# Kernel optimization log

Measured on AMD Instinct MI355X. Metric: run time of the kernel, lower is better.

## Reference

```python
import jax, jax.numpy as jnp
import numpy as np

BATCH, SEQ_LEN, ENC_IN = 16, 1024, 12
N_HIPPO, MODES, OUT_DIM = 256, 32, 5
MULTISCALE = [1, 2, 4]
EPS_VAR, EPS_AFF = 1e-5, 1e-10


def _transition_lmu(N):
    Q = np.arange(N, dtype=np.float64)
    R = (2 * Q + 1)[:, None]
    j, i = np.meshgrid(Q, Q)
    A = np.where(i < j, -1.0, (-1.0) ** (i - j + 1)) * R
    B = (-1.0) ** Q[:, None] * R
    return A, B


def _bilinear_discretize(A, B, dt):
    # scipy.signal.cont2discrete(..., method='bilinear')
    N = A.shape[0]
    I = np.eye(N)
    ima = I - (dt / 2.0) * A
    Ad = np.linalg.solve(ima, I + (dt / 2.0) * A)
    Bd = np.linalg.solve(ima, dt * B)
    return Ad, Bd.squeeze(-1)


def _eval_legendre(N, x):
    # P_n(x) for n=0..N-1 via three-term recurrence; returns (len(x), N)
    P = np.zeros((len(x), N), dtype=np.float64)
    P[:, 0] = 1.0
    if N > 1:
        P[:, 1] = x
    for n in range(1, N - 1):
        P[:, n + 1] = ((2 * n + 1) * x * P[:, n] - n * P[:, n - 1]) / (n + 1)
    return P


def setup_inputs() -> dict:
    key = jax.random.key(0)
    ks = jax.random.split(key, 8)
    A_list, B_list, E_list = [], [], []
    for mult in MULTISCALE:
        dt = 1.0 / SEQ_LEN / mult
        A, B = _transition_lmu(N_HIPPO)
        Ad, Bd = _bilinear_discretize(A, B, dt)
        vals = np.arange(0.0, 1.0, dt)
        ev = _eval_legendre(N_HIPPO, 1.0 - 2.0 * vals)  # (seq_len*mult, N)
        A_list.append(Ad); B_list.append(Bd); E_list.append(ev[-SEQ_LEN:, :])
    scale = 1.0 / (N_HIPPO * N_HIPPO)
    inp = {
        "x_enc": jax.random.normal(ks[0], (BATCH, SEQ_LEN, ENC_IN), jnp.float32),
        "affine_w": jnp.ones((1, 1, ENC_IN), jnp.float32),
        "affine_b": jnp.zeros((1, 1, ENC_IN), jnp.float32),
        "w_spec_re": scale * jax.random.uniform(ks[1], (len(MULTISCALE), N_HIPPO, N_HIPPO, MODES), jnp.float32),
        "w_spec_im": scale * jax.random.uniform(ks[2], (len(MULTISCALE), N_HIPPO, N_HIPPO, MODES), jnp.float32),
        "w_mlp": 0.3 * jax.random.normal(ks[3], (1, len(MULTISCALE)), jnp.float32),
        "b_mlp": jnp.zeros((1,), jnp.float32),
        "w_fc": 0.05 * jax.random.normal(ks[4], (OUT_DIM, ENC_IN), jnp.float32),
        "b_fc": jnp.zeros((OUT_DIM,), jnp.float32),
        "A_mats": jnp.asarray(np.stack(A_list), jnp.float32),   # (3, N, N)
        "B_vecs": jnp.asarray(np.stack(B_list), jnp.float32),   # (3, N)
        "eval_last": jnp.asarray(np.stack(E_list), jnp.float32),  # (3, seq_len, N)
    }
    return inp


def reference(x_enc, affine_w, affine_b, w_spec_re, w_spec_im, w_mlp, b_mlp,
              w_fc, b_fc, A_mats, B_vecs, eval_last):
    L = x_enc.shape[1]
    # RevIN-style normalization (means/stdev are detached in torch)
    means = jax.lax.stop_gradient(jnp.mean(x_enc, axis=1, keepdims=True))
    xc = x_enc - means
    stdev = jax.lax.stop_gradient(jnp.sqrt(jnp.var(xc, axis=1, keepdims=True) + EPS_VAR))
    x = xc / stdev * affine_w + affine_b          # (B, L, C)
    xt = jnp.transpose(x, (0, 2, 1))              # (B, C, L)
    xt_seq = jnp.moveaxis(xt, -1, 0)              # (L, B, C)
    w_spec = (w_spec_re + 1j * w_spec_im).astype(jnp.complex64)
    modes2 = w_spec.shape[-1]
    decs = []
    for s in range(len(MULTISCALE)):
        A, Bv = A_mats[s], B_vecs[s]
        def step(c, f):  # c: (B,C,N), f: (B,C)
            c = c @ A.T + f[..., None] * Bv
            return c, c
        c0 = jnp.zeros(xt.shape[:2] + (A.shape[0],), xt.dtype)
        _, cs = jax.lax.scan(step, c0, xt_seq)    # (L, B, C, N)
        x_in_c = jnp.transpose(cs, (1, 2, 3, 0))  # (B, C, N, L)
        x_ft = jnp.fft.rfft(x_in_c)               # (B, C, N, L//2+1)
        out_low = jnp.einsum('bjix,iox->bjox', x_ft[..., :modes2], w_spec[s])
        out_ft = jnp.pad(out_low, ((0, 0), (0, 0), (0, 0), (0, x_ft.shape[-1] - modes2)))
        out = jnp.fft.irfft(out_ft, n=L)          # (B, C, N, L)
        x_dec_c = out[..., L - 1]                 # (B, C, N)
        decs.append(x_dec_c @ eval_last[s].T)     # (B, C, L)
    xd = jnp.stack(decs, axis=-1)                 # (B, C, L, 3)
    xd = (xd @ w_mlp.T + b_mlp)[..., 0]           # (B, C, L)
    x_dec = jnp.transpose(xd, (0, 2, 1))          # (B, L, C)
    x_dec = (x_dec - affine_b) / (affine_w + EPS_AFF) * stdev + means
    feat = jnp.mean(jnp.transpose(x_dec, (0, 2, 1)), axis=-1)  # (B, C)
    return feat @ w_fc.T + b_fc                   # (B, OUT_DIM)
```

## Files before the change

kernel.cpp:

```cpp
#include <hip/hip_runtime.h>
#include <math.h>

#define LSEQ 1024
#define NB 16
#define NC 12
#define NH 256
#define NM 32
#define NS 3
#define TWO_PI 6.283185307179586f

#define NPL   8
#define PSTR  196608
#define VPSTR 786432

#define OFF_MEANS 0
#define OFF_STDEV 192
#define OFF_EPART 384
#define OFF_WT_RE 24960
#define OFF_WT_IM 49536
#define OFF_VP    74112
#define OFF_V     6365568
#define OFF_PP0   7152000
#define OFF_PP1   8724864
#define OFF_H     10297728

__device__ __forceinline__ float block_reduce_sum(float v, float* sbuf) {
  int t = threadIdx.x;
  sbuf[t] = v; __syncthreads();
  for (int off = 128; off > 0; off >>= 1) {
    if (t < off) sbuf[t] += sbuf[t + off];
    __syncthreads();
  }
  float r = sbuf[0];
  __syncthreads();
  return r;
}

__global__ __launch_bounds__(256) void k_front(const float* __restrict__ Bv,
                                               const float* __restrict__ ev,
                                               const float* __restrict__ b_fc,
                                               float* __restrict__ epart,
                                               float* __restrict__ Vp,
                                               float* __restrict__ H,
                                               float* __restrict__ out) {
  int blk = blockIdx.x;
  int t = threadIdx.x;
  if (blk < 96) {
    int s = blk >> 5, ch = blk & 31;
    float acc = 0.f;
    const float* base = ev + (size_t)s * LSEQ * NH + (size_t)ch * 32 * NH + t;
    for (int l = 0; l < 32; ++l) acc += base[(size_t)l * NH];
    epart[(size_t)blk * NH + t] = acc;
  } else if (blk == 96) {
    for (int pl = 0; pl < NPL; ++pl)
      for (int row = t; row < 768; row += 256)
        Vp[(size_t)pl * VPSTR + (size_t)row * LSEQ] = (pl == 0) ? Bv[row] : 0.0f;
  } else {
    for (int e = 0; e < 4; ++e) H[t + 256 * e] = 0.0f;
    if (t < NB * 5) out[t] = b_fc[t % 5];
  }
}

__device__ __forceinline__ void wtilde_task(int w, float* smem,
                                            const float* __restrict__ wre,
                                            const float* __restrict__ wim,
                                            const float* __restrict__ epart,
                                            float* __restrict__ wt_re,
                                            float* __restrict__ wt_im) {
  int s = w >> 8, i = w & 255;
  int t = threadIdx.x;
  float* ebs = smem;
  float* sr  = smem + 256;
  float* si2 = smem + 1280;
  float eb = 0.f;
  for (int ch = 0; ch < 32; ++ch) eb += epart[(s * 32 + ch) * 256 + t];
  ebs[t] = eb * (1.0f / LSEQ);
  __syncthreads();
  const float* br = wre + (size_t)(s * NH + i) * NH * NM;
  const float* bi = wim + (size_t)(s * NH + i) * NH * NM;
  float aR[4] = {0.f, 0.f, 0.f, 0.f}, aI[4] = {0.f, 0.f, 0.f, 0.f};
  #pragma unroll
  for (int it = 0; it < 8; ++it) {
    int o = (t >> 3) + 32 * it;
    float e = ebs[o];
    float4 vr = *(const float4*)(br + (size_t)t * 4 + 1024 * it);
    float4 vi = *(const float4*)(bi + (size_t)t * 4 + 1024 * it);
    aR[0] += e * vr.x; aR[1] += e * vr.y; aR[2] += e * vr.z; aR[3] += e * vr.w;
    aI[0] += e * vi.x; aI[1] += e * vi.y; aI[2] += e * vi.z; aI[3] += e * vi.w;
  }
  *(float4*)(sr + t * 4)  = make_float4(aR[0], aR[1], aR[2], aR[3]);
  *(float4*)(si2 + t * 4) = make_float4(aI[0], aI[1], aI[2], aI[3]);
  __syncthreads();
  if (t < 32) {
    float r = 0.f, im = 0.f;
    #pragma unroll
    for (int og = 0; og < 32; ++og) { r += sr[og * 32 + t]; im += si2[og * 32 + t]; }
    wt_re[(size_t)(s * NM + t) * NH + i] = r;
    wt_im[(size_t)(s * NM + t) * NH + i] = im;
  }
  __syncthreads();
}

#define FMA_ROW(r, av) { acc[r][0] += (av)*b4.x; acc[r][1] += (av)*b4.y; acc[r][2] += (av)*b4.z; acc[r][3] += (av)*b4.w; }

template<int ANP, int BNP>
__device__ __forceinline__ void gemm32(float* As, float* Bs,
                       const float* Abase, int apstr,
                       const float* Bbase, int bpstr, int bld, int colLimit,
                       int rowbase, int colbase, int kb,
                       float* outp, int outld, int outcol0, int outColLim) {
  const int tid = threadIdx.x;
  const int tx = tid & 15, ty = tid >> 4;
  const int kkA = tid & 31, rA = tid >> 5;
  const int jB = tid & 63, kB = tid >> 6;
  float acc[8][4];
  #pragma unroll
  for (int i = 0; i < 8; ++i)
    #pragma unroll
    for (int j = 0; j < 4; ++j) acc[i][j] = 0.f;

  #pragma unroll
  for (int p = 0; p < 16; ++p) {
    int row = rowbase + rA + 8 * p;
    float pv[ANP];
    #pragma unroll
    for (int pp = 0; pp < ANP; ++pp)
      pv[pp] = Abase[(size_t)pp * apstr + (size_t)row * 256 + kb + kkA];
    float v = pv[0];
    #pragma unroll
    for (int pp = 1; pp < ANP; ++pp) v += pv[pp];
    As[kkA * 132 + rA + 8 * p] = v;
  }
  #pragma unroll
  for (int q = 0; q < 8; ++q) {
    int kk = kB + 4 * q;
    int j = colbase + jB;
    float v = 0.f;
    if (j < colLimit) {
      float pv[BNP];
      #pragma unroll
      for (int pp = 0; pp < BNP; ++pp)
        pv[pp] = Bbase[(size_t)pp * bpstr + (size_t)(kb + kk) * bld + j];
      v = pv[0];
      #pragma unroll
      for (int pp = 1; pp < BNP; ++pp) v += pv[pp];
    }
    Bs[kk * 68 + jB] = v;
  }
  __syncthreads();
  #pragma unroll
  for (int kk = 0; kk < 32; ++kk) {
    float4 b4 = *(const float4*)(Bs + kk * 68 + tx * 4);
    float4 a0 = *(const float4*)(As + kk * 132 + ty * 8);
    float4 a1 = *(const float4*)(As + kk * 132 + ty * 8 + 4);
    FMA_ROW(0, a0.x) FMA_ROW(1, a0.y) FMA_ROW(2, a0.z) FMA_ROW(3, a0.w)
    FMA_ROW(4, a1.x) FMA_ROW(5, a1.y) FMA_ROW(6, a1.z) FMA_ROW(7, a1.w)
  }
  __syncthreads();
  if (colbase + 64 <= outColLim) {
    #pragma unroll
    for (int i = 0; i < 8; ++i) {
      int row = rowbase + ty * 8 + i;
      float4 st; st.x = acc[i][0]; st.y = acc[i][1]; st.z = acc[i][2]; st.w = acc[i][3];
      *(float4*)(outp + (size_t)row * outld + outcol0 + colbase + tx * 4) = st;
    }
  } else {
    #pragma unroll
    for (int i = 0; i < 8; ++i) {
      int row = rowbase + ty * 8 + i;
      #pragma unroll
      for (int j = 0; j < 4; ++j) {
        int c = colbase + tx * 4 + j;
        if (c < outColLim) outp[(size_t)row * outld + outcol0 + c] = acc[i][j];
      }
    }
  }
}

template<int ANP>
__global__ __launch_bounds__(256) void k_chain(const float* __restrict__ Pc,
                                               float* __restrict__ Pn,
                                               float* __restrict__ Vp,
                                               int m, int nSq, int ntct,
                                               const float* __restrict__ wre,
                                               const float* __restrict__ wim,
                                               const float* __restrict__ epart,
                                               float* __restrict__ wt_re,
                                               float* __restrict__ wt_im,
                                               int wstart, int wcount,
                                               const float* __restrict__ x,
                                               float* __restrict__ means,
                                               float* __restrict__ stdev,
                                               int statCount, int redCount,
                                               float* __restrict__ V) {
  __shared__ float smem[6608];
  float* As = smem;
  float* Bs = smem + 4224;
  const int blk = blockIdx.x;
  const int t = threadIdx.x;
  const int nExt = 48 * ntct;
  const int b0 = nSq + nExt;
  if (blk < nSq) {
    int slice = blk & 7, rest = blk >> 3;
    int t8 = rest & 7, s = rest >> 3;
    int rt = t8 & 1, ct = t8 >> 1;
    const float* Ab = Pc + (size_t)s * 65536;
    gemm32<ANP, ANP>(As, Bs, Ab, PSTR, Ab, PSTR, 256, 256,
           rt * 128, ct * 64, slice * 32,
           Pn + (size_t)slice * PSTR + (size_t)s * 65536, 256, 0, 256);
  } else if (blk < b0) {
    int e = blk - nSq;
    int slice = e & 7, rt = (e >> 3) & 1, rest2 = e >> 4;
    int ct = rest2 % ntct, s = rest2 / ntct;
    gemm32<ANP, NPL>(As, Bs, Pc + (size_t)s * 65536, PSTR,
           Vp + (size_t)s * 262144, VPSTR, 1024, m,
           rt * 128, ct * 64, slice * 32,
           Vp + (size_t)slice * VPSTR + (size_t)s * 262144, 1024, m, m);
  } else if (blk < b0 + wcount) {
    wtilde_task(wstart + (blk - b0), smem, wre, wim, epart, wt_re, wt_im);
  } else if (blk < b0 + wcount + statCount) {
    int bc = blk - b0 - wcount;
    int b = bc / NC, c = bc % NC;
    float* xs = smem;
    float* red = smem + 1024;
    for (int e = 0; e < 4; ++e) {
      int tau = t + 256 * e;
      xs[tau] = x[((size_t)b * LSEQ + tau) * NC + c];
    }
    __syncthreads();
    float p = 0.f;
    for (int e = 0; e < 4; ++e) p += xs[t + 256 * e];
    float sum = block_reduce_sum(p, red);
    float mean = sum * (1.0f / LSEQ);
    float q = 0.f;
    for (int e = 0; e < 4; ++e) { float d = xs[t + 256 * e] - mean; q += d * d; }
    float sq = block_reduce_sum(q, red);
    if (t == 0) {
      means[bc] = mean;
      stdev[bc] = sqrtf(sq * (1.0f / LSEQ) + 1e-5f);
    }
  } else if (blk < b0 + wcount + statCount + redCount) {
    int rid = blk - b0 - wcount - statCount;
    for (int e = 0; e < 2; ++e) {
      size_t idx = (size_t)rid * 1024 + e * 256 + t;
      float v = 0.f;
      #pragma unroll
      for (int pl = 0; pl < NPL; ++pl) v += Vp[(size_t)pl * VPSTR + idx];
      V[idx] = v;
    }
  }
}

__global__ __launch_bounds__(256) void k_reduceV2(const float* __restrict__ Vp,
                                                  float* __restrict__ V) {
  int t = threadIdx.x;
  for (int e = 0; e < 2; ++e) {
    size_t idx = (size_t)blockIdx.x * 1024 + 512 + e * 256 + t;
    float v = 0.f;
    #pragma unroll
    for (int pl = 0; pl < NPL; ++pl) v += Vp[(size_t)pl * VPSTR + idx];
    V[idx] = v;
  }
}

__global__ __launch_bounds__(256) void k_utscan(const float* __restrict__ wt_re,
                                                const float* __restrict__ wt_im,
                                                const float* __restrict__ V,
                                                const float* __restrict__ w_mlp,
                                                float* __restrict__ H) {
  int blk = blockIdx.x;
  int s = blk / NM, k = blk & 31;
  int t = threadIdx.x;
  __shared__ float sr[LSEQ], si_[LSEQ];
  __shared__ float cr[256], ci[256];
  const float* wr = wt_re + (size_t)blk * NH;
  const float* wi_ = wt_im + (size_t)blk * NH;
  const float* Vs = V + (size_t)s * NH * LSEQ;
  float ar[4] = {0.f, 0.f, 0.f, 0.f}, ai[4] = {0.f, 0.f, 0.f, 0.f};
  for (int i = 0; i < NH; ++i) {
    float a = wr[i], b = wi_[i];
    const float* vrow = Vs + (size_t)i * LSEQ + t;
    #pragma unroll
    for (int e = 0; e < 4; ++e) {
      float v = vrow[256 * e];
      ar[e] += a * v; ai[e] += b * v;
    }
  }
  for (int e = 0; e < 4; ++e) {
    int d = t + 256 * e;
    int frac = (k * d) & 1023;
    float ang = -(TWO_PI / 1024.0f) * (float)frac;
    float sn, csn; sincosf(ang, &sn, &csn);
    sr[d] = ar[e] * csn - ai[e] * sn;
    si_[d] = ar[e] * sn + ai[e] * csn;
  }
  __syncthreads();
  float lr[4], li[4], rr = 0.f, ii = 0.f;
  for (int e = 0; e < 4; ++e) {
    rr += sr[4 * t + e]; ii += si_[4 * t + e];
    lr[e] = rr; li[e] = ii;
  }
  cr[t] = rr; ci[t] = ii;
  __syncthreads();
  for (int off = 1; off < 256; off <<= 1) {
    float pr = 0.f, pi = 0.f;
    if (t >= off) { pr = cr[t - off]; pi = ci[t - off]; }
    __syncthreads();
    cr[t] += pr; ci[t] += pi;
    __syncthreads();
  }
  float offr = (t > 0) ? cr[t - 1] : 0.0f;
  float offi = (t > 0) ? ci[t - 1] : 0.0f;
  for (int e = 0; e < 4; ++e) {
    sr[4 * t + e] = lr[e] + offr;
    si_[4 * t + e] = li[e] + offi;
  }
  __syncthreads();
  float wm = w_mlp[s];
  float coef = wm * ((k == 0) ? 1.0f : 2.0f) * (1.0f / LSEQ);
  for (int e = 0; e < 4; ++e) {
    int tau = t + 256 * e;
    int mIdx = 1023 - tau;
    int frac = (k * (tau + 1)) & 1023;
    float ang = -(TWO_PI / 1024.0f) * (float)frac;
    float sn, csn; sincosf(ang, &sn, &csn);
    float val = coef * (sr[mIdx] * csn - si_[mIdx] * sn);
    atomicAdd(&H[tau], val);
  }
}

__global__ __launch_bounds__(256) void k_feat(const float* __restrict__ x,
                                              const float* __restrict__ means,
                                              const float* __restrict__ stdev,
                                              const float* __restrict__ aw,
                                              const float* __restrict__ ab,
                                              const float* __restrict__ b_mlp,
                                              const float* __restrict__ H,
                                              const float* __restrict__ w_fc,
                                              float* __restrict__ out) {
  int bc = blockIdx.x; int b = bc / NC, c = bc % NC;
  __shared__ float red[256];
  int t = threadIdx.x;
  float mn = means[bc], sd = stdev[bc];
  float w = aw[c], bb = ab[c];
  float acc = 0.f;
  for (int e = 0; e < 4; ++e) {
    int tau = t + 256 * e;
    float xv = x[((size_t)b * LSEQ + tau) * NC + c];
    float f = (xv - mn) / sd * w + bb;
    acc += f * H[tau];
  }
  float sum = block_reduce_sum(acc, red);
  if (t == 0) {
    float mr = sum + b_mlp[0];
    float featv = (mr - bb) / (w + 1e-10f) * sd + mn;
    #pragma unroll
    for (int d = 0; d < 5; ++d)
      atomicAdd(&out[b * 5 + d], featv * w_fc[d * NC + c]);
  }
}

extern "C" void kernel_launch(void* const* d_in, const int* in_sizes, int n_in,
                              void* d_out, int out_size, void* d_ws, size_t ws_size,
                              hipStream_t stream) {
  const float* x_enc   = (const float*)d_in[0];
  const float* aw      = (const float*)d_in[1];
  const float* ab      = (const float*)d_in[2];
  const float* wre     = (const float*)d_in[3];
  const float* wim     = (const float*)d_in[4];
  const float* w_mlp   = (const float*)d_in[5];
  const float* b_mlp   = (const float*)d_in[6];
  const float* w_fc    = (const float*)d_in[7];
  const float* b_fc    = (const float*)d_in[8];
  const float* A_mats  = (const float*)d_in[9];
  const float* B_vecs  = (const float*)d_in[10];
  const float* ev      = (const float*)d_in[11];

  float* ws    = (float*)d_ws;
  float* means = ws + OFF_MEANS;
  float* stdev = ws + OFF_STDEV;
  float* epart = ws + OFF_EPART;
  float* wt_re = ws + OFF_WT_RE;
  float* wt_im = ws + OFF_WT_IM;
  float* Vp    = ws + OFF_VP;
  float* V     = ws + OFF_V;
  float* PP0   = ws + OFF_PP0;
  float* PP1   = ws + OFF_PP1;
  float* H     = ws + OFF_H;
  float* out   = (float*)d_out;

  k_front<<<98, 256, 0, stream>>>(B_vecs, ev, b_fc, epart, Vp, H, out);

  static const int wst[5] = {0, 154, 308, 462, 616};
  static const int wcn[5] = {154, 154, 154, 154, 152};
  const float* Pc = A_mats;
  float* Pn = PP0;
  for (int si = 0; si < 10; ++si) {
    int m = 1 << si;
    int doSq = (si < 9);
    int nSq = doSq ? 192 : 0;
    int ntct = (m + 63) >> 6;
    int wstart = (si < 5) ? wst[si] : 0;
    int wcount = (si < 5) ? wcn[si] : 0;
    int statCount = (si == 0) ? 192 : 0;
    int redCount = (si == 9) ? 768 : 0;
    int grid = nSq + 48 * ntct + wcount + statCount + redCount;
    if (si == 0)
      k_chain<1><<<grid, 256, 0, stream>>>(Pc, Pn, Vp, m, nSq, ntct,
          wre, wim, epart, wt_re, wt_im, wstart, wcount,
          x_enc, means, stdev, statCount, redCount, V);
    else
      k_chain<NPL><<<grid, 256, 0, stream>>>(Pc, Pn, Vp, m, nSq, ntct,
          wre, wim, epart, wt_re, wt_im, wstart, wcount,
          x_enc, means, stdev, statCount, redCount, V);
    if (doSq) { Pc = Pn; Pn = (Pn == PP0) ? PP1 : PP0; }
  }

  k_reduceV2<<<768, 256, 0, stream>>>(Vp, V);
  k_utscan<<<NS * NM, 256, 0, stream>>>(wt_re, wt_im, V, w_mlp, H);
  k_feat<<<192, 256, 0, stream>>>(x_enc, means, stdev, aw, ab, b_mlp, H, w_fc, out);
}
```

Measured before the change: 172.8 us.

## Fold front-end setup into first chain launch and vectorize utscan loads

Removes the separate k_front launch. Its Legendre-sum, H/out init and Vp seeding work now runs as extra block roles inside the first k_chain launch, where columns 0 and 1 of V are computed directly with a small matrix-vector product instead of a GEMM extension. The wtilde tasks are shifted one step later so they read epart only after it has been produced. k_utscan now loads V with float4 and does the twiddle multiply in registers, skipping one shared-memory pass and a barrier. This saves one kernel launch and some shared traffic, but it changes V's column-to-thread mapping and adds more block roles to the chain kernel.

```diff
diff --git a/kernel.cpp b/kernel.cpp
--- a/kernel.cpp
+++ b/kernel.cpp
@@ -34,31 +34,6 @@
   float r = sbuf[0];
   __syncthreads();
   return r;
-}
-
-__global__ __launch_bounds__(256) void k_front(const float* __restrict__ Bv,
-                                               const float* __restrict__ ev,
-                                               const float* __restrict__ b_fc,
-                                               float* __restrict__ epart,
-                                               float* __restrict__ Vp,
-                                               float* __restrict__ H,
-                                               float* __restrict__ out) {
-  int blk = blockIdx.x;
-  int t = threadIdx.x;
-  if (blk < 96) {
-    int s = blk >> 5, ch = blk & 31;
-    float acc = 0.f;
-    const float* base = ev + (size_t)s * LSEQ * NH + (size_t)ch * 32 * NH + t;
-    for (int l = 0; l < 32; ++l) acc += base[(size_t)l * NH];
-    epart[(size_t)blk * NH + t] = acc;
-  } else if (blk == 96) {
-    for (int pl = 0; pl < NPL; ++pl)
-      for (int row = t; row < 768; row += 256)
-        Vp[(size_t)pl * VPSTR + (size_t)row * LSEQ] = (pl == 0) ? Bv[row] : 0.0f;
-  } else {
-    for (int e = 0; e < 4; ++e) H[t + 256 * e] = 0.0f;
-    if (t < NB * 5) out[t] = b_fc[t % 5];
-  }
 }
 
 __device__ __forceinline__ void wtilde_task(int w, float* smem,
@@ -184,7 +159,7 @@
                                                int m, int nSq, int ntct,
                                                const float* __restrict__ wre,
                                                const float* __restrict__ wim,
-                                               const float* __restrict__ epart,
+                                               const float* __restrict__ epart_c,
                                                float* __restrict__ wt_re,
                                                float* __restrict__ wt_im,
                                                int wstart, int wcount,
@@ -192,7 +167,16 @@
                                                float* __restrict__ means,
                                                float* __restrict__ stdev,
                                                int statCount, int redCount,
-                                               float* __restrict__ V) {
+                                               float* __restrict__ V,
+                                               const float* __restrict__ ev,
+                                               float* __restrict__ epart_w,
+                                               int epCount,
+                                               const float* __restrict__ Bv,
+                                               int v01Count,
+                                               const float* __restrict__ b_fc,
+                                               float* __restrict__ H,
+                                               float* __restrict__ out,
+                                               int hCount) {
   __shared__ float smem[6608];
   float* As = smem;
   float* Bs = smem + 4224;
@@ -200,6 +184,11 @@
   const int t = threadIdx.x;
   const int nExt = 48 * ntct;
   const int b0 = nSq + nExt;
+  const int b1 = b0 + wcount;
+  const int b2 = b1 + statCount;
+  const int b3 = b2 + redCount;
+  const int b4_ = b3 + epCount;
+  const int b5 = b4_ + v01Count;
   if (blk < nSq) {
     int slice = blk & 7, rest = blk >> 3;
     int t8 = rest & 7, s = rest >> 3;
@@ -216,10 +205,10 @@
            Vp + (size_t)s * 262144, VPSTR, 1024, m,
            rt * 128, ct * 64, slice * 32,
            Vp + (size_t)slice * VPSTR + (size_t)s * 262144, 1024, m, m);
-  } else if (blk < b0 + wcount) {
-    wtilde_task(wstart + (blk - b0), smem, wre, wim, epart, wt_re, wt_im);
-  } else if (blk < b0 + wcount + statCount) {
-    int bc = blk - b0 - wcount;
+  } else if (blk < b1) {
+    wtilde_task(wstart + (blk - b0), smem, wre, wim, epart_c, wt_re, wt_im);
+  } else if (blk < b2) {
+    int bc = blk - b1;
     int b = bc / NC, c = bc % NC;
     float* xs = smem;
     float* red = smem + 1024;
@@ -239,8 +228,8 @@
       means[bc] = mean;
       stdev[bc] = sqrtf(sq * (1.0f / LSEQ) + 1e-5f);
     }
-  } else if (blk < b0 + wcount + statCount + redCount) {
-    int rid = blk - b0 - wcount - statCount;
+  } else if (blk < b3) {
+    int rid = blk - b2;
     for (int e = 0; e < 2; ++e) {
       size_t idx = (size_t)rid * 1024 + e * 256 + t;
       float v = 0.f;
@@ -248,6 +237,42 @@
       for (int pl = 0; pl < NPL; ++pl) v += Vp[(size_t)pl * VPSTR + idx];
       V[idx] = v;
     }
+  } else if (blk < b4_) {
+    int bb = blk - b3;
+    int s = bb >> 5, ch = bb & 31;
+    float acc = 0.f;
+    const float* base = ev + (size_t)s * LSEQ * NH + (size_t)ch * 32 * NH + t;
+    for (int l = 0; l < 32; ++l) acc += base[(size_t)l * NH];
+    epart_w[(size_t)bb * NH + t] = acc;
+  } else if (blk < b5) {
+    int v = blk - b4_;
+    int s = v >> 1, half = v & 1;
+    float* bsh = smem;
+    float* psh = smem + 256;
+    bsh[t] = Bv[s * 256 + t];
+    __syncthreads();
+    int i = half * 128 + (t >> 1);
+    int k2 = (t & 1) * 128;
+    const float* Arow = Pc + (size_t)s * 65536 + (size_t)i * 256 + k2;
+    float acc = 0.f;
+    for (int kk = 0; kk < 128; ++kk) acc += Arow[kk] * bsh[k2 + kk];
+    psh[t] = acc;
+    __syncthreads();
+    if ((t & 1) == 0) {
+      int row = s * 256 + i;
+      Vp[(size_t)row * 1024 + 1] = psh[t] + psh[t + 1];
+      Vp[(size_t)row * 1024] = bsh[i];
+    }
+    for (int z = t; z < 7 * 128 * 2; z += 256) {
+      int pl = 1 + (z >> 8);
+      int rr2 = (z >> 1) & 127;
+      int col = z & 1;
+      int row = s * 256 + half * 128 + rr2;
+      Vp[(size_t)pl * VPSTR + (size_t)row * 1024 + col] = 0.f;
+    }
+  } else if (blk < b5 + hCount) {
+    for (int e = 0; e < 4; ++e) H[t + 256 * e] = 0.0f;
+    if (t < NB * 5) out[t] = b_fc[t % 5];
   }
 }
 
@@ -279,25 +304,22 @@
   float ar[4] = {0.f, 0.f, 0.f, 0.f}, ai[4] = {0.f, 0.f, 0.f, 0.f};
   for (int i = 0; i < NH; ++i) {
     float a = wr[i], b = wi_[i];
-    const float* vrow = Vs + (size_t)i * LSEQ + t;
-    #pragma unroll
-    for (int e = 0; e < 4; ++e) {
-      float v = vrow[256 * e];
-      ar[e] += a * v; ai[e] += b * v;
-    }
-  }
+    float4 v4 = *(const float4*)(Vs + (size_t)i * LSEQ + 4 * t);
+    ar[0] += a * v4.x; ai[0] += b * v4.x;
+    ar[1] += a * v4.y; ai[1] += b * v4.y;
+    ar[2] += a * v4.z; ai[2] += b * v4.z;
+    ar[3] += a * v4.w; ai[3] += b * v4.w;
+  }
+  float lr[4], li[4], rr = 0.f, ii = 0.f;
+  #pragma unroll
   for (int e = 0; e < 4; ++e) {
-    int d = t + 256 * e;
+    int d = 4 * t + e;
     int frac = (k * d) & 1023;
     float ang = -(TWO_PI / 1024.0f) * (float)frac;
     float sn, csn; sincosf(ang, &sn, &csn);
-    sr[d] = ar[e] * csn - ai[e] * sn;
-    si_[d] = ar[e] * sn + ai[e] * csn;
-  }
-  __syncthreads();
-  float lr[4], li[4], rr = 0.f, ii = 0.f;
-  for (int e = 0; e < 4; ++e) {
-    rr += sr[4 * t + e]; ii += si_[4 * t + e];
+    float tr = ar[e] * csn - ai[e] * sn;
+    float ti = ar[e] * sn + ai[e] * csn;
+    rr += tr; ii += ti;
     lr[e] = rr; li[e] = ii;
   }
   cr[t] = rr; ci[t] = ii;
@@ -311,6 +333,7 @@
   }
   float offr = (t > 0) ? cr[t - 1] : 0.0f;
   float offi = (t > 0) ? ci[t - 1] : 0.0f;
+  #pragma unroll
   for (int e = 0; e < 4; ++e) {
     sr[4 * t + e] = lr[e] + offr;
     si_[4 * t + e] = li[e] + offi;
@@ -389,30 +412,33 @@
   float* H     = ws + OFF_H;
   float* out   = (float*)d_out;
 
-  k_front<<<98, 256, 0, stream>>>(B_vecs, ev, b_fc, epart, Vp, H, out);
-
+  static const int wcn[5] = {154, 154, 154, 154, 152};
   static const int wst[5] = {0, 154, 308, 462, 616};
-  static const int wcn[5] = {154, 154, 154, 154, 152};
   const float* Pc = A_mats;
   float* Pn = PP0;
   for (int si = 0; si < 10; ++si) {
     int m = 1 << si;
     int doSq = (si < 9);
     int nSq = doSq ? 192 : 0;
-    int ntct = (m + 63) >> 6;
-    int wstart = (si < 5) ? wst[si] : 0;
-    int wcount = (si < 5) ? wcn[si] : 0;
+    int ntct = (si == 0) ? 0 : ((m + 63) >> 6);
+    int wstart = (si >= 1 && si <= 5) ? wst[si - 1] : 0;
+    int wcount = (si >= 1 && si <= 5) ? wcn[si - 1] : 0;
     int statCount = (si == 0) ? 192 : 0;
     int redCount = (si == 9) ? 768 : 0;
-    int grid = nSq + 48 * ntct + wcount + statCount + redCount;
+    int epCount = (si == 0) ? 96 : 0;
+    int v01Count = (si == 0) ? 6 : 0;
+    int hCount = (si == 0) ? 1 : 0;
+    int grid = nSq + 48 * ntct + wcount + statCount + redCount + epCount + v01Count + hCount;
     if (si == 0)
       k_chain<1><<<grid, 256, 0, stream>>>(Pc, Pn, Vp, m, nSq, ntct,
           wre, wim, epart, wt_re, wt_im, wstart, wcount,
-          x_enc, means, stdev, statCount, redCount, V);
+          x_enc, means, stdev, statCount, redCount, V,
+          ev, epart, epCount, B_vecs, v01Count, b_fc, H, out, hCount);
     else
       k_chain<NPL><<<grid, 256, 0, stream>>>(Pc, Pn, Vp, m, nSq, ntct,
           wre, wim, epart, wt_re, wt_im, wstart, wcount,
-          x_enc, means, stdev, statCount, redCount, V);
+          x_enc, means, stdev, statCount, redCount, V,
+          ev, epart, epCount, B_vecs, v01Count, b_fc, H, out, hCount);
     if (doSq) { Pc = Pn; Pn = (Pn == PP0) ? PP1 : PP0; }
   }
 
```

Measured after the change: 161.2 us. 1.07x faster.
